# Performance work log

Measured on AMD Instinct MI355X. Metric: run time of the kernel, lower is better.

## Reference

```python
import jax, jax.numpy as jnp
import numpy as np

B = 512      # batch = envs * nagents
M = 32       # nmodels
NAG = 8      # nagents
H = 256      # hidsz
NACT = 16    # nactions


def _lm(x, W, b, ids):
    # LinearMulti: per-example weight selected by model id.
    # x: [B, I], W: [M, I, O], b: [M, O], ids: [B] -> [B, O]
    return jnp.einsum('bi,bio->bo', x, W[ids]) + b[ids]


def setup_inputs() -> dict:
    key = jax.random.key(0)
    ks = jax.random.split(key, 16)
    s = 0.02
    return {
        'comm_in': jax.random.normal(ks[0], (B, NAG, H), jnp.float32),
        'inp': jnp.zeros((B, 1), jnp.int32),  # Embedding table has 1 row -> only index 0 valid
        'prev_hid': jax.random.normal(ks[1], (B, H), jnp.float32),
        'prev_cell': jnp.zeros((B, H), jnp.float32),  # unused in rnn branch, kept for signature fidelity
        'model_ids': jax.random.randint(ks[2], (B,), 0, M),
        # comm2hid LinearMulti (comm_encoder): hidsz -> hidsz
        'Wc': jax.random.normal(ks[3], (M, H, H), jnp.float32) * s,
        'bc': jax.random.normal(ks[4], (M, H), jnp.float32) * s,
        # rnn LinearMulti: hidsz -> hidsz
        'Wr': jax.random.normal(ks[5], (M, H, H), jnp.float32) * s,
        'br': jax.random.normal(ks[6], (M, H), jnp.float32) * s,
        # action LinearMulti: hidsz -> nactions
        'Wa': jax.random.normal(ks[7], (M, H, NACT), jnp.float32) * s,
        'ba': jax.random.normal(ks[8], (M, NACT), jnp.float32) * s,
        # baseline LinearMulti: hidsz -> 1
        'Wb': jax.random.normal(ks[9], (M, H, 1), jnp.float32) * s,
        'bb': jax.random.normal(ks[10], (M, 1), jnp.float32) * s,
        # comm_out LinearMulti (fully_connected): hidsz -> hidsz * nagents
        'Wo': jax.random.normal(ks[11], (M, H, H * NAG), jnp.float32) * s,
        'bo': jax.random.normal(ks[12], (M, H * NAG), jnp.float32) * s,
        # Encoder: Embedding(1, hidsz) + bias
        'lut': jax.random.normal(ks[13], (1, H), jnp.float32) * s,
        'enc_bias': jax.random.normal(ks[14], (H,), jnp.float32) * s,
    }


def reference(comm_in, inp, prev_hid, prev_cell, model_ids,
              Wc, bc, Wr, br, Wa, ba, Wb, bb, Wo, bo, lut, enc_bias):
    # __comm2hid: sum agent messages, then model-id-routed linear
    comm2hid = _lm(jnp.sum(comm_in, axis=1), Wc, bc, model_ids)  # [B, H]
    # Encoder: embedding lookup, sum over token dim, add bias
    enc = jnp.sum(lut[inp], axis=1) + enc_bias                   # [B, H]
    # _rnn: sum of encoder, routed recurrent linear, and comm; tanh gate
    hidstate = jnp.tanh(enc + _lm(prev_hid, Wr, br, model_ids) + comm2hid)
    # __action
    action_prob = jax.nn.softmax(_lm(hidstate, Wa, ba, model_ids), axis=-1)  # [B, NACT]
    baseline = _lm(hidstate, Wb, bb, model_ids)                              # [B, 1]
    # __comm_out (fully_connected): routed linear then divide by nagents-1
    comm_out = _lm(hidstate, Wo, bo, model_ids) / (NAG - 1)                  # [B, H*NAG]
    return (action_prob, baseline, hidstate, comm_out)
```

## Files before the change

### kernel.cpp

```cpp
#include <hip/hip_runtime.h>


constexpr int Bn = 512, Mn = 32, NAGn = 8, Hn = 256, NACTn = 16;
constexpr int On = Hn * NAGn;
constexpr int En = 32;
constexpr int EW = 8;
constexpr int XS = 40;
constexpr int XS2 = 36;

__device__ __forceinline__ void gl_lds16(const float* g, float* l) {
  __builtin_amdgcn_global_load_lds(
      (const __attribute__((address_space(1))) void*)g,
      (__attribute__((address_space(3))) void*)l, 16, 0, 0);
}

__device__ __forceinline__ int build_group_det(const int* __restrict__ ids,
                                               int m, int* lst, int* segc,
                                               int tid) {
  int w = tid >> 6, lane = tid & 63;
  if (tid < En) lst[tid] = -1;
  unsigned long long msk[2];
#pragma unroll
  for (int p = 0; p < 2; p++) {
    int i = (w * 2 + p) * 64 + lane;
    msk[p] = __ballot(ids[i] == m);
  }
  if (lane == 0) {
    segc[w * 2 + 0] = __popcll(msk[0]);
    segc[w * 2 + 1] = __popcll(msk[1]);
  }
  __syncthreads();
  int tot = 0;
#pragma unroll
  for (int q = 0; q < 8; q++) tot += segc[q];
#pragma unroll
  for (int p = 0; p < 2; p++) {
    int s = w * 2 + p;
    int pre = 0;
    for (int q = 0; q < 8; q++)
      if (q < s) pre += segc[q];
    int i = s * 64 + lane;
    if ((msk[p] >> lane) & 1ull) {
      int rank = pre + __popcll(msk[p] & ((1ull << lane) - 1ull));
      if (rank < En) lst[rank] = i;
    }
  }
  __syncthreads();
  return tot;
}

__global__ __launch_bounds__(256) void k_linh(
    const float* __restrict__ Wc, const float* __restrict__ Wr,
    const float* __restrict__ comm_in, const float* __restrict__ prev_hid,
    const int* __restrict__ ids, const int* __restrict__ inp,
    const float* __restrict__ lut, const float* __restrict__ enc_bias,
    const float* __restrict__ bc, const float* __restrict__ br,
    float* __restrict__ hid) {
  int m = blockIdx.x, ct = blockIdx.y;
  int tid = threadIdx.x, w = tid >> 6, lane = tid & 63;
  __shared__ int lst[En];
  __shared__ int segc[8];
  __shared__ alignas(16) float xs[512 * XS2];
  __shared__ alignas(16) float wbuf[4][128 * 32];

  int cnt = build_group_det(ids, m, lst, segc, tid);
  if (cnt == 0) return;

  auto issue_tile = [&](int t) {
    const float* base = ((t < 2) ? Wc : Wr) + (size_t)m * Hn * Hn +
                        (size_t)((t & 1) * 128) * Hn + ct * 32;
    float* dst = wbuf[t];
#pragma unroll
    for (int q = 0; q < 4; q++) {
      int c = w * 4 + q;
      int r = c * 8 + (lane >> 3);
      gl_lds16(base + (size_t)r * Hn + (lane & 7) * 4, dst + c * 256);
    }
  };
  issue_tile(0);
  issue_tile(1);

  {
    int k = tid;
#pragma unroll 2
    for (int j = 0; j < En; j++) {
      int e = lst[j];
      float vc = 0.f, vr = 0.f;
      if (e >= 0) {
        const float* cp = comm_in + (size_t)e * (NAGn * Hn) + k;
#pragma unroll
        for (int a = 0; a < NAGn; a++) vc += cp[a * Hn];
        vr = prev_hid[(size_t)e * Hn + k];
      }
      xs[k * XS2 + j] = vc;
      xs[(256 + k) * XS2 + j] = vr;
    }
  }
  issue_tile(2);
  issue_tile(3);

  __syncthreads();
  __builtin_amdgcn_sched_barrier(0);

  int j0 = w * EW;
  int kpar = lane >> 5, col = lane & 31;
  float acc[EW];
#pragma unroll
  for (int i = 0; i < EW; i++) acc[i] = 0.f;

#pragma unroll
  for (int t = 0; t < 4; t++) {
    const float* wb = wbuf[t] + col;
    const float* xb = xs + (size_t)(t * 128 + kpar) * XS2 + j0;
#pragma unroll 8
    for (int kk = 0; kk < 64; kk++) {
      float wv = wb[(2 * kk + kpar) * 32];
      float4 xa = *(const float4*)(xb + (2 * kk) * XS2);
      float4 xc = *(const float4*)(xb + (2 * kk) * XS2 + 4);
      acc[0] += xa.x * wv; acc[1] += xa.y * wv;
      acc[2] += xa.z * wv; acc[3] += xa.w * wv;
      acc[4] += xc.x * wv; acc[5] += xc.y * wv;
      acc[6] += xc.z * wv; acc[7] += xc.w * wv;
    }
  }

#pragma unroll
  for (int i = 0; i < EW; i++) acc[i] += __shfl_xor(acc[i], 32);
  if (lane < 32) {
    int cg = ct * 32 + lane;
    float bsum = bc[m * Hn + cg] + br[m * Hn + cg] + enc_bias[cg];
#pragma unroll
    for (int i = 0; i < EW; i++) {
      int e = lst[j0 + i];
      if (e < 0) continue;
      float h = tanhf(acc[i] + bsum + lut[(size_t)inp[e] * Hn + cg]);
      hid[(size_t)e * Hn + cg] = h;
    }
  }
}

__global__ __launch_bounds__(256) void k_outh(
    const float* __restrict__ Wo, const float* __restrict__ bo,
    const float* __restrict__ hid, const int* __restrict__ ids,
    const float* __restrict__ Wa, const float* __restrict__ ba,
    const float* __restrict__ Wb, const float* __restrict__ bb,
    float* __restrict__ aprob, float* __restrict__ bl,
    float* __restrict__ comm_out) {
  int ct = blockIdx.x, m = blockIdx.y;
  int tid = threadIdx.x, w = tid >> 6, lane = tid & 63;
  __shared__ int lst[En];
  __shared__ int segc[8];
  __shared__ alignas(16) float xs[Hn * XS];
  __shared__ alignas(16) float wbuf[3][16 * 128];

  int cnt = build_group_det(ids, m, lst, segc, tid);
  if (cnt == 0) return;

  const float* wsrc = Wo + (size_t)m * Hn * On + ct * 128;
#pragma unroll
  for (int tt = 0; tt < 2; tt++) {
#pragma unroll
    for (int q = 0; q < 2; q++) {
      int c = w * 2 + q;
      int row = tt * 16 + c * 2 + (lane >> 5);
      gl_lds16(wsrc + (size_t)row * On + (lane & 31) * 4, wbuf[tt] + c * 256);
    }
  }

  for (int j = 0; j < En; j++) {
    int e = lst[j];
    float v = (e >= 0) ? hid[(size_t)e * Hn + tid] : 0.f;
    xs[tid * XS + j] = v;
  }
  asm volatile("s_waitcnt lgkmcnt(0)" ::: "memory");
  __builtin_amdgcn_s_barrier();
  __builtin_amdgcn_sched_barrier(0);

  {
    int jt = (w == 0) ? ct : (w == 1) ? ct + 16 : -1;
    int e = (jt >= 0) ? lst[jt] : -1;
    if (e >= 0) {
      int l = lane, o = l & 15, kk = l >> 4;
      const float* wap = Wa + (size_t)m * Hn * NACTn + l;
      float al = 0.f;
      for (int w16 = 0; w16 < 4; w16++) {
        float wv[16], hv[16];
#pragma unroll
        for (int il = 0; il < 16; il++) wv[il] = wap[(w16 * 16 + il) * 64];
#pragma unroll
        for (int il = 0; il < 16; il++)
          hv[il] = xs[(w16 * 64 + il * 4 + kk) * XS + jt];
#pragma unroll
        for (int il = 0; il < 16; il++) al += wv[il] * hv[il];
      }
      al += __shfl_xor(al, 16);
      al += __shfl_xor(al, 32);
      al += ba[m * NACTn + o];

      float mx = al;
      mx = fmaxf(mx, __shfl_xor(mx, 1));
      mx = fmaxf(mx, __shfl_xor(mx, 2));
      mx = fmaxf(mx, __shfl_xor(mx, 4));
      mx = fmaxf(mx, __shfl_xor(mx, 8));
      float ex = expf(al - mx);
      float sm = ex;
      sm += __shfl_xor(sm, 1);
      sm += __shfl_xor(sm, 2);
      sm += __shfl_xor(sm, 4);
      sm += __shfl_xor(sm, 8);
      if (l < 16) aprob[e * NACTn + l] = ex / sm;

      float pb = 0.f;
      const float* wbp = Wb + (size_t)m * Hn;
      {
        float wv[4], hv[4];
#pragma unroll
        for (int k2 = 0; k2 < 4; k2++) {
          wv[k2] = wbp[l + k2 * 64];
          hv[k2] = xs[(l + k2 * 64) * XS + jt];
        }
#pragma unroll
        for (int k2 = 0; k2 < 4; k2++) pb += wv[k2] * hv[k2];
      }
      pb += __shfl_xor(pb, 1);
      pb += __shfl_xor(pb, 2);
      pb += __shfl_xor(pb, 4);
      pb += __shfl_xor(pb, 8);
      pb += __shfl_xor(pb, 16);
      pb += __shfl_xor(pb, 32);
      if (l == 0) bl[e] = pb + bb[m];
    }
  }

  int j0 = w * EW;
  float2 acc[EW];
#pragma unroll
  for (int j = 0; j < EW; j++) acc[j] = make_float2(0.f, 0.f);

  for (int t = 0; t < 16; t++) {
    if (t < 14) {
      const float* ws2 = wsrc + (size_t)(t + 2) * 16 * On;
#pragma unroll
      for (int q = 0; q < 2; q++) {
        int c = w * 2 + q;
        int row = c * 2 + (lane >> 5);
        gl_lds16(ws2 + (size_t)row * On + (lane & 31) * 4,
                 wbuf[(t + 2) % 3] + c * 256);
      }
      asm volatile("s_waitcnt vmcnt(4)" ::: "memory");
    } else if (t == 14) {
      asm volatile("s_waitcnt vmcnt(2)" ::: "memory");
    } else {
      asm volatile("s_waitcnt vmcnt(0)" ::: "memory");
    }
    __builtin_amdgcn_s_barrier();
    __builtin_amdgcn_sched_barrier(0);
    const float* wb = wbuf[t % 3] + lane * 2;
    const float* xb = xs + (size_t)(t * 16) * XS + j0;
#pragma unroll 8
    for (int k = 0; k < 16; k++) {
      float2 wv = *(const float2*)(wb + k * 128);
      float4 xa = *(const float4*)(xb + k * XS);
      float4 xc = *(const float4*)(xb + k * XS + 4);
      acc[0].x += xa.x * wv.x; acc[0].y += xa.x * wv.y;
      acc[1].x += xa.y * wv.x; acc[1].y += xa.y * wv.y;
      acc[2].x += xa.z * wv.x; acc[2].y += xa.z * wv.y;
      acc[3].x += xa.w * wv.x; acc[3].y += xa.w * wv.y;
      acc[4].x += xc.x * wv.x; acc[4].y += xc.x * wv.y;
      acc[5].x += xc.y * wv.x; acc[5].y += xc.y * wv.y;
      acc[6].x += xc.z * wv.x; acc[6].y += xc.z * wv.y;
      acc[7].x += xc.w * wv.x; acc[7].y += xc.w * wv.y;
    }
    __builtin_amdgcn_sched_barrier(0);
    __builtin_amdgcn_s_barrier();
    __builtin_amdgcn_sched_barrier(0);
  }
  float2 bv = *(const float2*)(bo + (size_t)m * On + ct * 128 + lane * 2);
  const float inv = 1.f / 7.f;
#pragma unroll
  for (int jj = 0; jj < EW; jj++) {
    int e = lst[j0 + jj];
    if (e < 0) continue;
    float2 o;
    o.x = (acc[jj].x + bv.x) * inv;
    o.y = (acc[jj].y + bv.y) * inv;
    *(float2*)(comm_out + (size_t)e * On + ct * 128 + lane * 2) = o;
  }
}

extern "C" void kernel_launch(void* const* d_in, const int* in_sizes, int n_in,
                              void* d_out, int out_size, void* d_ws, size_t ws_size,
                              hipStream_t stream) {
  const float* comm_in  = (const float*)d_in[0];
  const int*   inp      = (const int*)d_in[1];
  const float* prev_hid = (const float*)d_in[2];
  const int*   ids      = (const int*)d_in[4];
  const float* Wc = (const float*)d_in[5];
  const float* bc = (const float*)d_in[6];
  const float* Wr = (const float*)d_in[7];
  const float* br = (const float*)d_in[8];
  const float* Wa = (const float*)d_in[9];
  const float* ba = (const float*)d_in[10];
  const float* Wb = (const float*)d_in[11];
  const float* bb = (const float*)d_in[12];
  const float* Wo = (const float*)d_in[13];
  const float* bo = (const float*)d_in[14];
  const float* lut      = (const float*)d_in[15];
  const float* enc_bias = (const float*)d_in[16];

  float* out      = (float*)d_out;
  float* aprob    = out;
  float* bl       = out + Bn * NACTn;
  float* hid      = out + Bn * NACTn + Bn;
  float* comm_out = hid + Bn * Hn;

  (void)d_ws; (void)ws_size;

  k_linh<<<dim3(Mn, 8), 256, 0, stream>>>(Wc, Wr, comm_in, prev_hid, ids, inp,
                                          lut, enc_bias, bc, br, hid);
  k_outh<<<dim3(16, Mn), 256, 0, stream>>>(Wo, bo, hid, ids, Wa, ba, Wb, bb,
                                           aprob, bl, comm_out);
}
```

Measured before the change: 180.6 us.

## Split k_linh over example halves and deepen k_outh weight prefetch pipeline

k_linh gains a third grid dimension that splits each model's 32-example group into two halves of 16. The smaller per-block LDS footprint (two weight buffers and a narrower activation tile) should raise occupancy and parallelism, and the Wr tiles are now fetched after the Wc pass, reusing the two buffers. The activation gather also moves to float4 loads. k_outh goes from a 3-deep to a 4-deep LDS ring with a vmcnt schedule to match, issuing the next tile after the end-of-iteration barrier, which hides more of the Wo load latency at the cost of more LDS and the Wc/Wr weights being read twice.

```diff
diff --git a/kernel.cpp b/kernel.cpp
--- a/kernel.cpp
+++ b/kernel.cpp
@@ -6,7 +6,7 @@
 constexpr int En = 32;
 constexpr int EW = 8;
 constexpr int XS = 40;
-constexpr int XS2 = 36;
+constexpr int XS3 = 20;
 
 __device__ __forceinline__ void gl_lds16(const float* g, float* l) {
   __builtin_amdgcn_global_load_lds(
@@ -56,20 +56,20 @@
     const float* __restrict__ lut, const float* __restrict__ enc_bias,
     const float* __restrict__ bc, const float* __restrict__ br,
     float* __restrict__ hid) {
-  int m = blockIdx.x, ct = blockIdx.y;
+  int m = blockIdx.x, ct = blockIdx.y, jh = blockIdx.z;
   int tid = threadIdx.x, w = tid >> 6, lane = tid & 63;
   __shared__ int lst[En];
   __shared__ int segc[8];
-  __shared__ alignas(16) float xs[512 * XS2];
-  __shared__ alignas(16) float wbuf[4][128 * 32];
+  __shared__ alignas(16) float xs[512 * XS3];
+  __shared__ alignas(16) float wbuf[2][128 * 32];
 
   int cnt = build_group_det(ids, m, lst, segc, tid);
   if (cnt == 0) return;
 
-  auto issue_tile = [&](int t) {
+  auto issue_tile = [&](int t, int buf) {
     const float* base = ((t < 2) ? Wc : Wr) + (size_t)m * Hn * Hn +
                         (size_t)((t & 1) * 128) * Hn + ct * 32;
-    float* dst = wbuf[t];
+    float* dst = wbuf[buf];
 #pragma unroll
     for (int q = 0; q < 4; q++) {
       int c = w * 4 + q;
@@ -77,61 +77,80 @@
       gl_lds16(base + (size_t)r * Hn + (lane & 7) * 4, dst + c * 256);
     }
   };
-  issue_tile(0);
-  issue_tile(1);
+  issue_tile(0, 0);
+  issue_tile(1, 1);
 
   {
-    int k = tid;
-#pragma unroll 2
-    for (int j = 0; j < En; j++) {
-      int e = lst[j];
-      float vc = 0.f, vr = 0.f;
+    int kq = tid >> 2, jg = tid & 3;
+#pragma unroll
+    for (int jj = 0; jj < 4; jj++) {
+      int j = jg + 4 * jj;
+      int e = lst[jh * 16 + j];
+      float4 vc = make_float4(0.f, 0.f, 0.f, 0.f);
+      float4 vr = vc;
       if (e >= 0) {
-        const float* cp = comm_in + (size_t)e * (NAGn * Hn) + k;
-#pragma unroll
-        for (int a = 0; a < NAGn; a++) vc += cp[a * Hn];
-        vr = prev_hid[(size_t)e * Hn + k];
+        const float4* cp =
+            (const float4*)(comm_in + (size_t)e * (NAGn * Hn)) + kq;
+#pragma unroll
+        for (int a = 0; a < NAGn; a++) {
+          float4 t = cp[a * (Hn / 4)];
+          vc.x += t.x; vc.y += t.y; vc.z += t.z; vc.w += t.w;
+        }
+        vr = *((const float4*)(prev_hid + (size_t)e * Hn) + kq);
       }
-      xs[k * XS2 + j] = vc;
-      xs[(256 + k) * XS2 + j] = vr;
-    }
-  }
-  issue_tile(2);
-  issue_tile(3);
-
-  __syncthreads();
-  __builtin_amdgcn_sched_barrier(0);
-
-  int j0 = w * EW;
+      int r = kq * 4;
+      xs[(r + 0) * XS3 + j] = vc.x;
+      xs[(r + 1) * XS3 + j] = vc.y;
+      xs[(r + 2) * XS3 + j] = vc.z;
+      xs[(r + 3) * XS3 + j] = vc.w;
+      xs[(256 + r + 0) * XS3 + j] = vr.x;
+      xs[(256 + r + 1) * XS3 + j] = vr.y;
+      xs[(256 + r + 2) * XS3 + j] = vr.z;
+      xs[(256 + r + 3) * XS3 + j] = vr.w;
+    }
+  }
+
+  int j0 = w * 4;
   int kpar = lane >> 5, col = lane & 31;
-  float acc[EW];
-#pragma unroll
-  for (int i = 0; i < EW; i++) acc[i] = 0.f;
-
-#pragma unroll
-  for (int t = 0; t < 4; t++) {
-    const float* wb = wbuf[t] + col;
-    const float* xb = xs + (size_t)(t * 128 + kpar) * XS2 + j0;
+  float acc[4];
+#pragma unroll
+  for (int i = 0; i < 4; i++) acc[i] = 0.f;
+
+#pragma unroll
+  for (int half = 0; half < 2; half++) {
+    __syncthreads();
+    __builtin_amdgcn_sched_barrier(0);
+#pragma unroll
+    for (int tt = 0; tt < 2; tt++) {
+      int t = half * 2 + tt;
+      const float* wb = wbuf[tt] + col;
+      const float* xb = xs + (size_t)(t * 128 + kpar) * XS3 + j0;
 #pragma unroll 8
-    for (int kk = 0; kk < 64; kk++) {
-      float wv = wb[(2 * kk + kpar) * 32];
-      float4 xa = *(const float4*)(xb + (2 * kk) * XS2);
-      float4 xc = *(const float4*)(xb + (2 * kk) * XS2 + 4);
-      acc[0] += xa.x * wv; acc[1] += xa.y * wv;
-      acc[2] += xa.z * wv; acc[3] += xa.w * wv;
-      acc[4] += xc.x * wv; acc[5] += xc.y * wv;
-      acc[6] += xc.z * wv; acc[7] += xc.w * wv;
-    }
-  }
-
-#pragma unroll
-  for (int i = 0; i < EW; i++) acc[i] += __shfl_xor(acc[i], 32);
+      for (int kk = 0; kk < 64; kk++) {
+        float wv = wb[(2 * kk + kpar) * 32];
+        float4 xa = *(const float4*)(xb + (2 * kk) * XS3);
+        acc[0] += xa.x * wv;
+        acc[1] += xa.y * wv;
+        acc[2] += xa.z * wv;
+        acc[3] += xa.w * wv;
+      }
+    }
+    if (half == 0) {
+      __builtin_amdgcn_sched_barrier(0);
+      __syncthreads();
+      issue_tile(2, 0);
+      issue_tile(3, 1);
+    }
+  }
+
+#pragma unroll
+  for (int i = 0; i < 4; i++) acc[i] += __shfl_xor(acc[i], 32);
   if (lane < 32) {
     int cg = ct * 32 + lane;
     float bsum = bc[m * Hn + cg] + br[m * Hn + cg] + enc_bias[cg];
 #pragma unroll
-    for (int i = 0; i < EW; i++) {
-      int e = lst[j0 + i];
+    for (int i = 0; i < 4; i++) {
+      int e = lst[jh * 16 + j0 + i];
       if (e < 0) continue;
       float h = tanhf(acc[i] + bsum + lut[(size_t)inp[e] * Hn + cg]);
       hid[(size_t)e * Hn + cg] = h;
@@ -151,21 +170,24 @@
   __shared__ int lst[En];
   __shared__ int segc[8];
   __shared__ alignas(16) float xs[Hn * XS];
-  __shared__ alignas(16) float wbuf[3][16 * 128];
+  __shared__ alignas(16) float wbuf[4][16 * 128];
 
   int cnt = build_group_det(ids, m, lst, segc, tid);
   if (cnt == 0) return;
 
   const float* wsrc = Wo + (size_t)m * Hn * On + ct * 128;
-#pragma unroll
-  for (int tt = 0; tt < 2; tt++) {
+  auto issue_tile = [&](int t) {
+    const float* ws2 = wsrc + (size_t)t * 16 * On;
 #pragma unroll
     for (int q = 0; q < 2; q++) {
       int c = w * 2 + q;
-      int row = tt * 16 + c * 2 + (lane >> 5);
-      gl_lds16(wsrc + (size_t)row * On + (lane & 31) * 4, wbuf[tt] + c * 256);
-    }
-  }
+      int row = c * 2 + (lane >> 5);
+      gl_lds16(ws2 + (size_t)row * On + (lane & 31) * 4,
+               wbuf[t & 3] + c * 256);
+    }
+  };
+#pragma unroll
+  for (int t = 0; t < 4; t++) issue_tile(t);
 
   for (int j = 0; j < En; j++) {
     int e = lst[j];
@@ -238,15 +260,9 @@
   for (int j = 0; j < EW; j++) acc[j] = make_float2(0.f, 0.f);
 
   for (int t = 0; t < 16; t++) {
-    if (t < 14) {
-      const float* ws2 = wsrc + (size_t)(t + 2) * 16 * On;
-#pragma unroll
-      for (int q = 0; q < 2; q++) {
-        int c = w * 2 + q;
-        int row = c * 2 + (lane >> 5);
-        gl_lds16(ws2 + (size_t)row * On + (lane & 31) * 4,
-                 wbuf[(t + 2) % 3] + c * 256);
-      }
+    if (t <= 12) {
+      asm volatile("s_waitcnt vmcnt(6)" ::: "memory");
+    } else if (t == 13) {
       asm volatile("s_waitcnt vmcnt(4)" ::: "memory");
     } else if (t == 14) {
       asm volatile("s_waitcnt vmcnt(2)" ::: "memory");
@@ -255,7 +271,7 @@
     }
     __builtin_amdgcn_s_barrier();
     __builtin_amdgcn_sched_barrier(0);
-    const float* wb = wbuf[t % 3] + lane * 2;
+    const float* wb = wbuf[t & 3] + lane * 2;
     const float* xb = xs + (size_t)(t * 16) * XS + j0;
 #pragma unroll 8
     for (int k = 0; k < 16; k++) {
@@ -274,6 +290,7 @@
     __builtin_amdgcn_sched_barrier(0);
     __builtin_amdgcn_s_barrier();
     __builtin_amdgcn_sched_barrier(0);
+    if (t <= 11) issue_tile(t + 4);
   }
   float2 bv = *(const float2*)(bo + (size_t)m * On + ct * 128 + lane * 2);
   const float inv = 1.f / 7.f;
@@ -316,8 +333,8 @@
 
   (void)d_ws; (void)ws_size;
 
-  k_linh<<<dim3(Mn, 8), 256, 0, stream>>>(Wc, Wr, comm_in, prev_hid, ids, inp,
-                                          lut, enc_bias, bc, br, hid);
+  k_linh<<<dim3(Mn, 8, 2), 256, 0, stream>>>(Wc, Wr, comm_in, prev_hid, ids,
+                                             inp, lut, enc_bias, bc, br, hid);
   k_outh<<<dim3(16, Mn), 256, 0, stream>>>(Wo, bo, hid, ids, Wa, ba, Wb, bb,
                                            aprob, bl, comm_out);
 }
```

Measured after the change: 170.7 us. 5.5% less time.

## Fuse hidden-state and comm_out kernels into one per-model 512-thread kernel

Applied to the files above, without the earlier changes.

Merges the two launches into a single kernel with grid (models, 8) and 512 threads. Each block recomputes the full hidden state for its model group (all 256 columns) in LDS and then streams its 256-column slice of Wo, so the intermediate hidden state never round-trips through global memory and the second launch disappears. The cost is that each of the 8 column-tile blocks redundantly streams the full Wc and Wr for its model, and the grid shrinks from 512 to 256 blocks, which may reduce parallelism for the dominant Wo stream.

```diff
diff --git a/kernel.cpp b/kernel.cpp
--- a/kernel.cpp
+++ b/kernel.cpp
@@ -4,9 +4,7 @@
 constexpr int Bn = 512, Mn = 32, NAGn = 8, Hn = 256, NACTn = 16;
 constexpr int On = Hn * NAGn;
 constexpr int En = 32;
-constexpr int EW = 8;
-constexpr int XS = 40;
-constexpr int XS2 = 36;
+constexpr int XSa = 36;
 
 __device__ __forceinline__ void gl_lds16(const float* g, float* l) {
   __builtin_amdgcn_global_load_lds(
@@ -19,167 +17,186 @@
                                                int tid) {
   int w = tid >> 6, lane = tid & 63;
   if (tid < En) lst[tid] = -1;
-  unsigned long long msk[2];
-#pragma unroll
-  for (int p = 0; p < 2; p++) {
-    int i = (w * 2 + p) * 64 + lane;
-    msk[p] = __ballot(ids[i] == m);
-  }
-  if (lane == 0) {
-    segc[w * 2 + 0] = __popcll(msk[0]);
-    segc[w * 2 + 1] = __popcll(msk[1]);
-  }
+  unsigned long long msk = __ballot(ids[tid] == m);
+  if (lane == 0) segc[w] = __popcll(msk);
   __syncthreads();
   int tot = 0;
 #pragma unroll
   for (int q = 0; q < 8; q++) tot += segc[q];
-#pragma unroll
-  for (int p = 0; p < 2; p++) {
-    int s = w * 2 + p;
-    int pre = 0;
-    for (int q = 0; q < 8; q++)
-      if (q < s) pre += segc[q];
-    int i = s * 64 + lane;
-    if ((msk[p] >> lane) & 1ull) {
-      int rank = pre + __popcll(msk[p] & ((1ull << lane) - 1ull));
-      if (rank < En) lst[rank] = i;
-    }
+  int pre = 0;
+#pragma unroll
+  for (int q = 0; q < 8; q++)
+    if (q < w) pre += segc[q];
+  if ((msk >> lane) & 1ull) {
+    int rank = pre + __popcll(msk & ((1ull << lane) - 1ull));
+    if (rank < En) lst[rank] = tid;
   }
   __syncthreads();
   return tot;
 }
 
-__global__ __launch_bounds__(256) void k_linh(
+__global__ __launch_bounds__(512) void k_fused(
     const float* __restrict__ Wc, const float* __restrict__ Wr,
-    const float* __restrict__ comm_in, const float* __restrict__ prev_hid,
-    const int* __restrict__ ids, const int* __restrict__ inp,
-    const float* __restrict__ lut, const float* __restrict__ enc_bias,
-    const float* __restrict__ bc, const float* __restrict__ br,
-    float* __restrict__ hid) {
+    const float* __restrict__ Wo, const float* __restrict__ comm_in,
+    const float* __restrict__ prev_hid, const int* __restrict__ ids,
+    const int* __restrict__ inp, const float* __restrict__ lut,
+    const float* __restrict__ enc_bias, const float* __restrict__ bc,
+    const float* __restrict__ br, const float* __restrict__ bo,
+    const float* __restrict__ Wa, const float* __restrict__ ba,
+    const float* __restrict__ Wb, const float* __restrict__ bb,
+    float* __restrict__ hid, float* __restrict__ aprob,
+    float* __restrict__ bl, float* __restrict__ comm_out) {
   int m = blockIdx.x, ct = blockIdx.y;
   int tid = threadIdx.x, w = tid >> 6, lane = tid & 63;
   __shared__ int lst[En];
   __shared__ int segc[8];
-  __shared__ alignas(16) float xs[512 * XS2];
-  __shared__ alignas(16) float wbuf[4][128 * 32];
+  __shared__ alignas(16) float xs1[256 * XSa];
+  __shared__ alignas(16) float xs2[256 * XSa];
+  __shared__ alignas(16) float wbuf[4][16 * 256];
 
   int cnt = build_group_det(ids, m, lst, segc, tid);
   if (cnt == 0) return;
 
-  auto issue_tile = [&](int t) {
-    const float* base = ((t < 2) ? Wc : Wr) + (size_t)m * Hn * Hn +
-                        (size_t)((t & 1) * 128) * Hn + ct * 32;
-    float* dst = wbuf[t];
-#pragma unroll
-    for (int q = 0; q < 4; q++) {
-      int c = w * 4 + q;
-      int r = c * 8 + (lane >> 3);
-      gl_lds16(base + (size_t)r * Hn + (lane & 7) * 4, dst + c * 256);
+  auto issue_tile = [&](const float* base, size_t rstride, int t) {
+#pragma unroll
+    for (int q = 0; q < 2; q++) {
+      int r = w * 2 + q;
+      gl_lds16(base + (size_t)(t * 16 + r) * rstride + lane * 4,
+               wbuf[t & 3] + r * 256);
     }
   };
-  issue_tile(0);
-  issue_tile(1);
+
+  int cp = 2 * (lane & 15);
+  int jo = (lane >> 4) * 8;
+  auto comp_tile = [&](const float* xsrc, int t, float2* acc) {
+    const float* wb = wbuf[t & 3] + w * 32 + cp;
+    const float* xb = xsrc + (size_t)(t * 16) * XSa + jo;
+#pragma unroll 8
+    for (int k = 0; k < 16; k++) {
+      float2 wv = *(const float2*)(wb + k * 256);
+      float4 xa = *(const float4*)(xb + k * XSa);
+      float4 xc = *(const float4*)(xb + k * XSa + 4);
+      acc[0].x += xa.x * wv.x; acc[0].y += xa.x * wv.y;
+      acc[1].x += xa.y * wv.x; acc[1].y += xa.y * wv.y;
+      acc[2].x += xa.z * wv.x; acc[2].y += xa.z * wv.y;
+      acc[3].x += xa.w * wv.x; acc[3].y += xa.w * wv.y;
+      acc[4].x += xc.x * wv.x; acc[4].y += xc.x * wv.y;
+      acc[5].x += xc.y * wv.x; acc[5].y += xc.y * wv.y;
+      acc[6].x += xc.z * wv.x; acc[6].y += xc.z * wv.y;
+      acc[7].x += xc.w * wv.x; acc[7].y += xc.w * wv.y;
+    }
+  };
+
+  auto stream16 = [&](const float* base, size_t rstride, const float* xsrc,
+                      float2* acc) {
+    for (int t = 0; t < 16; t++) {
+      if (t <= 12)
+        asm volatile("s_waitcnt vmcnt(6)" ::: "memory");
+      else if (t == 13)
+        asm volatile("s_waitcnt vmcnt(4)" ::: "memory");
+      else if (t == 14)
+        asm volatile("s_waitcnt vmcnt(2)" ::: "memory");
+      else
+        asm volatile("s_waitcnt vmcnt(0)" ::: "memory");
+      __builtin_amdgcn_s_barrier();
+      __builtin_amdgcn_sched_barrier(0);
+      comp_tile(xsrc, t, acc);
+      __builtin_amdgcn_sched_barrier(0);
+      __builtin_amdgcn_s_barrier();
+      __builtin_amdgcn_sched_barrier(0);
+      if (t <= 11) issue_tile(base, rstride, t + 4);
+    }
+  };
+
+  const float* WcB = Wc + (size_t)m * Hn * Hn;
+  const float* WrB = Wr + (size_t)m * Hn * Hn;
+#pragma unroll
+  for (int t = 0; t < 4; t++) issue_tile(WcB, Hn, t);
 
   {
-    int k = tid;
-#pragma unroll 2
-    for (int j = 0; j < En; j++) {
+    int kq = tid >> 3, jg = tid & 7;
+#pragma unroll
+    for (int jx = 0; jx < 4; jx++) {
+      int j = jg * 4 + jx;
       int e = lst[j];
-      float vc = 0.f, vr = 0.f;
+      float4 vc = make_float4(0.f, 0.f, 0.f, 0.f);
       if (e >= 0) {
-        const float* cp = comm_in + (size_t)e * (NAGn * Hn) + k;
-#pragma unroll
-        for (int a = 0; a < NAGn; a++) vc += cp[a * Hn];
-        vr = prev_hid[(size_t)e * Hn + k];
+        const float4* cpp =
+            (const float4*)(comm_in + (size_t)e * (NAGn * Hn)) + kq;
+#pragma unroll
+        for (int a = 0; a < NAGn; a++) {
+          float4 tv = cpp[a * (Hn / 4)];
+          vc.x += tv.x; vc.y += tv.y; vc.z += tv.z; vc.w += tv.w;
+        }
       }
-      xs[k * XS2 + j] = vc;
-      xs[(256 + k) * XS2 + j] = vr;
-    }
-  }
-  issue_tile(2);
-  issue_tile(3);
-
-  __syncthreads();
-  __builtin_amdgcn_sched_barrier(0);
-
-  int j0 = w * EW;
-  int kpar = lane >> 5, col = lane & 31;
-  float acc[EW];
-#pragma unroll
-  for (int i = 0; i < EW; i++) acc[i] = 0.f;
-
-#pragma unroll
-  for (int t = 0; t < 4; t++) {
-    const float* wb = wbuf[t] + col;
-    const float* xb = xs + (size_t)(t * 128 + kpar) * XS2 + j0;
-#pragma unroll 8
-    for (int kk = 0; kk < 64; kk++) {
-      float wv = wb[(2 * kk + kpar) * 32];
-      float4 xa = *(const float4*)(xb + (2 * kk) * XS2);
-      float4 xc = *(const float4*)(xb + (2 * kk) * XS2 + 4);
-      acc[0] += xa.x * wv; acc[1] += xa.y * wv;
-      acc[2] += xa.z * wv; acc[3] += xa.w * wv;
-      acc[4] += xc.x * wv; acc[5] += xc.y * wv;
-      acc[6] += xc.z * wv; acc[7] += xc.w * wv;
-    }
-  }
-
-#pragma unroll
-  for (int i = 0; i < EW; i++) acc[i] += __shfl_xor(acc[i], 32);
-  if (lane < 32) {
-    int cg = ct * 32 + lane;
-    float bsum = bc[m * Hn + cg] + br[m * Hn + cg] + enc_bias[cg];
-#pragma unroll
-    for (int i = 0; i < EW; i++) {
-      int e = lst[j0 + i];
+      int r = kq * 4;
+      xs1[(r + 0) * XSa + j] = vc.x;
+      xs1[(r + 1) * XSa + j] = vc.y;
+      xs1[(r + 2) * XSa + j] = vc.z;
+      xs1[(r + 3) * XSa + j] = vc.w;
+    }
+  }
+  __syncthreads();
+
+  float2 acc[8];
+#pragma unroll
+  for (int i = 0; i < 8; i++) acc[i] = make_float2(0.f, 0.f);
+  stream16(WcB, Hn, xs1, acc);
+
+#pragma unroll
+  for (int t = 0; t < 4; t++) issue_tile(WrB, Hn, t);
+  {
+    int kq = tid >> 3, jg = tid & 7;
+#pragma unroll
+    for (int jx = 0; jx < 4; jx++) {
+      int j = jg * 4 + jx;
+      int e = lst[j];
+      float4 vr = make_float4(0.f, 0.f, 0.f, 0.f);
+      if (e >= 0) vr = *((const float4*)(prev_hid + (size_t)e * Hn) + kq);
+      int r = kq * 4;
+      xs1[(r + 0) * XSa + j] = vr.x;
+      xs1[(r + 1) * XSa + j] = vr.y;
+      xs1[(r + 2) * XSa + j] = vr.z;
+      xs1[(r + 3) * XSa + j] = vr.w;
+    }
+  }
+  __syncthreads();
+  stream16(WrB, Hn, xs1, acc);
+
+  int c0 = w * 32 + cp;
+  float2 bsum;
+  bsum.x = bc[m * Hn + c0] + br[m * Hn + c0] + enc_bias[c0];
+  bsum.y = bc[m * Hn + c0 + 1] + br[m * Hn + c0 + 1] + enc_bias[c0 + 1];
+#pragma unroll
+  for (int i = 0; i < 8; i++) {
+    int j = jo + i, e = lst[j];
+    float hx = 0.f, hy = 0.f;
+    if (e >= 0) {
+      const float* lr = lut + (size_t)inp[e] * Hn;
+      hx = tanhf(acc[i].x + bsum.x + lr[c0]);
+      hy = tanhf(acc[i].y + bsum.y + lr[c0 + 1]);
+    }
+    xs2[(c0) * XSa + j] = hx;
+    xs2[(c0 + 1) * XSa + j] = hy;
+  }
+  __syncthreads();
+
+  const float* WoB = Wo + (size_t)m * Hn * On + ct * 256;
+#pragma unroll
+  for (int t = 0; t < 4; t++) issue_tile(WoB, On, t);
+
+  if (ct == 0) {
+#pragma unroll 4
+    for (int jj = 0; jj < 16; jj++) {
+      int j = jj * 2 + (tid >> 8);
+      int k = tid & 255;
+      int e = lst[j];
+      if (e >= 0) hid[(size_t)e * Hn + k] = xs2[k * XSa + j];
+    }
+    for (int s = 0; s < 4; s++) {
+      int jt = w * 4 + s;
+      int e = lst[jt];
       if (e < 0) continue;
-      float h = tanhf(acc[i] + bsum + lut[(size_t)inp[e] * Hn + cg]);
-      hid[(size_t)e * Hn + cg] = h;
-    }
-  }
-}
-
-__global__ __launch_bounds__(256) void k_outh(
-    const float* __restrict__ Wo, const float* __restrict__ bo,
-    const float* __restrict__ hid, const int* __restrict__ ids,
-    const float* __restrict__ Wa, const float* __restrict__ ba,
-    const float* __restrict__ Wb, const float* __restrict__ bb,
-    float* __restrict__ aprob, float* __restrict__ bl,
-    float* __restrict__ comm_out) {
-  int ct = blockIdx.x, m = blockIdx.y;
-  int tid = threadIdx.x, w = tid >> 6, lane = tid & 63;
-  __shared__ int lst[En];
-  __shared__ int segc[8];
-  __shared__ alignas(16) float xs[Hn * XS];
-  __shared__ alignas(16) float wbuf[3][16 * 128];
-
-  int cnt = build_group_det(ids, m, lst, segc, tid);
-  if (cnt == 0) return;
-
-  const float* wsrc = Wo + (size_t)m * Hn * On + ct * 128;
-#pragma unroll
-  for (int tt = 0; tt < 2; tt++) {
-#pragma unroll
-    for (int q = 0; q < 2; q++) {
-      int c = w * 2 + q;
-      int row = tt * 16 + c * 2 + (lane >> 5);
-      gl_lds16(wsrc + (size_t)row * On + (lane & 31) * 4, wbuf[tt] + c * 256);
-    }
-  }
-
-  for (int j = 0; j < En; j++) {
-    int e = lst[j];
-    float v = (e >= 0) ? hid[(size_t)e * Hn + tid] : 0.f;
-    xs[tid * XS + j] = v;
-  }
-  asm volatile("s_waitcnt lgkmcnt(0)" ::: "memory");
-  __builtin_amdgcn_s_barrier();
-  __builtin_amdgcn_sched_barrier(0);
-
-  {
-    int jt = (w == 0) ? ct : (w == 1) ? ct + 16 : -1;
-    int e = (jt >= 0) ? lst[jt] : -1;
-    if (e >= 0) {
       int l = lane, o = l & 15, kk = l >> 4;
       const float* wap = Wa + (size_t)m * Hn * NACTn + l;
       float al = 0.f;
@@ -189,7 +206,7 @@
         for (int il = 0; il < 16; il++) wv[il] = wap[(w16 * 16 + il) * 64];
 #pragma unroll
         for (int il = 0; il < 16; il++)
-          hv[il] = xs[(w16 * 64 + il * 4 + kk) * XS + jt];
+          hv[il] = xs2[(w16 * 64 + il * 4 + kk) * XSa + jt];
 #pragma unroll
         for (int il = 0; il < 16; il++) al += wv[il] * hv[il];
       }
@@ -217,7 +234,7 @@
 #pragma unroll
         for (int k2 = 0; k2 < 4; k2++) {
           wv[k2] = wbp[l + k2 * 64];
-          hv[k2] = xs[(l + k2 * 64) * XS + jt];
+          hv[k2] = xs2[(l + k2 * 64) * XSa + jt];
         }
 #pragma unroll
         for (int k2 = 0; k2 < 4; k2++) pb += wv[k2] * hv[k2];
@@ -232,59 +249,22 @@
     }
   }
 
-  int j0 = w * EW;
-  float2 acc[EW];
-#pragma unroll
-  for (int j = 0; j < EW; j++) acc[j] = make_float2(0.f, 0.f);
-
-  for (int t = 0; t < 16; t++) {
-    if (t < 14) {
-      const float* ws2 = wsrc + (size_t)(t + 2) * 16 * On;
-#pragma unroll
-      for (int q = 0; q < 2; q++) {
-        int c = w * 2 + q;
-        int row = c * 2 + (lane >> 5);
-        gl_lds16(ws2 + (size_t)row * On + (lane & 31) * 4,
-                 wbuf[(t + 2) % 3] + c * 256);
-      }
-      asm volatile("s_waitcnt vmcnt(4)" ::: "memory");
-    } else if (t == 14) {
-      asm volatile("s_waitcnt vmcnt(2)" ::: "memory");
-    } else {
-      asm volatile("s_waitcnt vmcnt(0)" ::: "memory");
-    }
-    __builtin_amdgcn_s_barrier();
-    __builtin_amdgcn_sched_barrier(0);
-    const float* wb = wbuf[t % 3] + lane * 2;
-    const float* xb = xs + (size_t)(t * 16) * XS + j0;
-#pragma unroll 8
-    for (int k = 0; k < 16; k++) {
-      float2 wv = *(const float2*)(wb + k * 128);
-      float4 xa = *(const float4*)(xb + k * XS);
-      float4 xc = *(const float4*)(xb + k * XS + 4);
-      acc[0].x += xa.x * wv.x; acc[0].y += xa.x * wv.y;
-      acc[1].x += xa.y * wv.x; acc[1].y += xa.y * wv.y;
-      acc[2].x += xa.z * wv.x; acc[2].y += xa.z * wv.y;
-      acc[3].x += xa.w * wv.x; acc[3].y += xa.w * wv.y;
-      acc[4].x += xc.x * wv.x; acc[4].y += xc.x * wv.y;
-      acc[5].x += xc.y * wv.x; acc[5].y += xc.y * wv.y;
-      acc[6].x += xc.z * wv.x; acc[6].y += xc.z * wv.y;
-      acc[7].x += xc.w * wv.x; acc[7].y += xc.w * wv.y;
-    }
-    __builtin_amdgcn_sched_barrier(0);
-    __builtin_amdgcn_s_barrier();
-    __builtin_amdgcn_sched_barrier(0);
-  }
-  float2 bv = *(const float2*)(bo + (size_t)m * On + ct * 128 + lane * 2);
+  float2 acc2[8];
+#pragma unroll
+  for (int i = 0; i < 8; i++) acc2[i] = make_float2(0.f, 0.f);
+  stream16(WoB, On, xs2, acc2);
+
+  int cg = ct * 256 + c0;
+  float2 bv = *(const float2*)(bo + (size_t)m * On + cg);
   const float inv = 1.f / 7.f;
 #pragma unroll
-  for (int jj = 0; jj < EW; jj++) {
-    int e = lst[j0 + jj];
+  for (int i = 0; i < 8; i++) {
+    int e = lst[jo + i];
     if (e < 0) continue;
     float2 o;
-    o.x = (acc[jj].x + bv.x) * inv;
-    o.y = (acc[jj].y + bv.y) * inv;
-    *(float2*)(comm_out + (size_t)e * On + ct * 128 + lane * 2) = o;
+    o.x = (acc2[i].x + bv.x) * inv;
+    o.y = (acc2[i].y + bv.y) * inv;
+    *(float2*)(comm_out + (size_t)e * On + cg) = o;
   }
 }
 
@@ -316,8 +296,7 @@
 
   (void)d_ws; (void)ws_size;
 
-  k_linh<<<dim3(Mn, 8), 256, 0, stream>>>(Wc, Wr, comm_in, prev_hid, ids, inp,
-                                          lut, enc_bias, bc, br, hid);
-  k_outh<<<dim3(16, Mn), 256, 0, stream>>>(Wo, bo, hid, ids, Wa, ba, Wb, bb,
-                                           aprob, bl, comm_out);
+  k_fused<<<dim3(Mn, 8), 512, 0, stream>>>(
+      Wc, Wr, Wo, comm_in, prev_hid, ids, inp, lut, enc_bias, bc, br, bo,
+      Wa, ba, Wb, bb, hid, aprob, bl, comm_out);
 }
```

New measurement: 217.2 us. +20.2%, slower.
